# Kernel tuning notes

Measured on AMD Instinct MI355X. Metric: run time of the kernel, lower is better.

## Reference

```python
import jax, jax.numpy as jnp
import numpy as np

B, S, D, H, K, L, NS, NT = 32, 512, 1024, 512, 16, 16, 16, 16
SMOOTH = 0.1
EPS = 1e-8


def setup_inputs() -> dict:
    key = jax.random.key(0)
    ks = jax.random.split(key, 16)
    hidden_layers = jax.random.normal(ks[0], (B, S, D), jnp.float32)
    span_start = jax.random.randint(ks[1], (B, K), 0, S - L).astype(jnp.int32)
    span_idx = span_start[..., None] + jnp.arange(L, dtype=jnp.int32)  # [B,K,L] in-range
    span_mask = jnp.ones((B, K, L), jnp.float32)
    span_end = span_start + (L - 1)
    length = jnp.full((B,), S, jnp.int32)
    slot_emb = jax.random.normal(ks[2], (B, K, D), jnp.float32)
    tgt_slot_embs = jax.random.normal(ks[3], (NT, D), jnp.float32)
    src_slot_ids = jax.random.randint(ks[4], (B, K), 0, NS).astype(jnp.int32)
    sc = 0.02
    p = {
        'Wih_f': jax.random.normal(ks[5], (4 * H, D)) * sc,
        'Whh_f': jax.random.normal(ks[6], (4 * H, H)) * sc,
        'bih_f': jnp.zeros((4 * H,)), 'bhh_f': jnp.zeros((4 * H,)),
        'Wih_b': jax.random.normal(ks[7], (4 * H, D)) * sc,
        'Whh_b': jax.random.normal(ks[8], (4 * H, H)) * sc,
        'bih_b': jnp.zeros((4 * H,)), 'bhh_b': jnp.zeros((4 * H,)),
        # slot_name_projection_for_slot / _for_context are eye-initialized with zero bias
        'Wps1': jnp.eye(D), 'bps1': jnp.zeros((D,)),
        'Wps2': jnp.eye(D), 'bps2': jnp.zeros((D,)),
        'Wpc1': jnp.eye(D), 'bpc1': jnp.zeros((D,)),
        'Wpc2': jnp.eye(D), 'bpc2': jnp.zeros((D,)),
    }
    inp = dict(hidden_layers=hidden_layers, span_idx=span_idx, span_mask=span_mask,
               span_start=span_start, span_end=span_end, length=length,
               slot_emb=slot_emb, tgt_slot_embs=tgt_slot_embs, src_slot_ids=src_slot_ids)
    inp.update(p)
    return inp


def _lstm_dir(x, m, Wih, Whh, bih, bhh):
    # x: [N,L,D], m: [N,L]; masked steps carry state through, emit 0
    N = x.shape[0]
    h0 = jnp.zeros((N, H), x.dtype)
    c0 = jnp.zeros((N, H), x.dtype)

    def step(carry, xm):
        h, c = carry
        xt, mt = xm
        g = xt @ Wih.T + h @ Whh.T + (bih + bhh)
        i, f, gg, o = jnp.split(g, 4, axis=-1)  # torch gate order i,f,g,o
        cn = jax.nn.sigmoid(f) * c + jax.nn.sigmoid(i) * jnp.tanh(gg)
        hn = jax.nn.sigmoid(o) * jnp.tanh(cn)
        mt = mt[:, None]
        h = mt * hn + (1.0 - mt) * h
        c = mt * cn + (1.0 - mt) * c
        return (h, c), h * mt

    _, ys = jax.lax.scan(step, (h0, c0), (jnp.swapaxes(x, 0, 1), m.T))
    return jnp.swapaxes(ys, 0, 1)  # [N,L,H]


def _mlp(x, W1, b1, W2, b2):
    # Linear -> Tanh -> (Dropout eval=identity) -> Linear
    return jnp.tanh(x @ W1.T + b1) @ W2.T + b2


def reference(hidden_layers, span_idx, span_mask, span_start, span_end, length,
              slot_emb, tgt_slot_embs, src_slot_ids,
              Wih_f, Whh_f, bih_f, bhh_f, Wih_b, Whh_b, bih_b, bhh_b,
              Wps1, bps1, Wps2, bps2, Wpc1, bpc1, Wpc2, bpc2):
    # gather span tokens: [B,K,L,D]
    spans = hidden_layers[jnp.arange(B)[:, None, None], span_idx]
    x = spans.reshape(B * K, L, D)
    m = span_mask.reshape(B * K, L)
    hf = _lstm_dir(x, m, Wih_f, Whh_f, bih_f, bhh_f)
    hb = _lstm_dir(x[:, ::-1], m[:, ::-1], Wih_b, Whh_b, bih_b, bhh_b)[:, ::-1]
    out = jnp.concatenate([hf, hb], axis=-1)           # [BK,L,2H]
    slot_feats = out.sum(axis=1).reshape(B, K, 2 * H)  # sum-pool over span

    # context attention (faithful to source: returns attn @ hidden, no softmax)
    sf = jax.lax.stop_gradient(slot_feats)
    pos = jnp.arange(S)
    cmask = (pos[None, None, :] < span_start[..., None]) | \
            ((pos[None, None, :] > span_end[..., None]) & (pos[None, None, :] < length[:, None, None]))
    attn = jnp.einsum('bkd,bsd->bks', sf, hidden_layers) * cmask.astype(hidden_layers.dtype)
    context = jnp.einsum('bks,bsd->bkd', attn, hidden_layers)  # [B,K,D]

    # smooth labels via projected slot-name embeddings (all detached in source)
    s_cat = jnp.concatenate([_mlp(slot_emb, Wps1, bps1, Wps2, bps2),
                             _mlp(slot_emb, Wpc1, bpc1, Wpc2, bpc2)], axis=-1)  # [B,K,2D]
    t_cat = jnp.concatenate([_mlp(tgt_slot_embs, Wps1, bps1, Wps2, bps2),
                             _mlp(tgt_slot_embs, Wpc1, bpc1, Wpc2, bpc2)], axis=-1)  # [NT,2D]
    s_cat = jax.lax.stop_gradient(s_cat)
    t_cat = jax.lax.stop_gradient(t_cat)
    sn = jnp.maximum(jnp.linalg.norm(s_cat, axis=-1), EPS)
    tn = jnp.maximum(jnp.linalg.norm(t_cat, axis=-1), EPS)
    sim = jnp.einsum('bkd,td->bkt', s_cat, t_cat) / (sn[..., None] * tn[None, None, :])
    sim = sim / sim.sum(axis=-1, keepdims=True) * (1.0 - SMOOTH)
    one_hot = jax.nn.one_hot(src_slot_ids, NS, dtype=sim.dtype) * SMOOTH
    labels = jnp.concatenate([one_hot, sim], axis=-1)  # [B,K,NS+NT]

    return jnp.concatenate([slot_feats, context, labels], axis=-1)  # [B,K,2H+D+NS+NT]
```

## Files before the change

kernel.cpp:

```cpp
#include <hip/hip_runtime.h>
#include <cstdio>

#define B_ 32
#define S_ 512
#define D_ 1024
#define H_ 512
#define K_ 16
#define L_ 16
#define NT_ 16
#define NSEQ 512
#define XROWS 8192
#define G4H 2048
#define OUTC 2080
#define MROWS 528

typedef unsigned short u16;
typedef __bf16 bf16x8 __attribute__((ext_vector_type(8)));
typedef float f32x4 __attribute__((ext_vector_type(4)));

__device__ inline u16 f2b(float f) {
  union { float f; unsigned u; } x; x.f = f;
  unsigned r = x.u + 0x7FFFu + ((x.u >> 16) & 1u);
  return (u16)(r >> 16);
}
__device__ inline float b2f(u16 h) {
  union { unsigned u; float f; } c; c.u = ((unsigned)h) << 16;
  return c.f;
}
__device__ inline float sigf(float x) { return 1.0f / (1.0f + expf(-x)); }
__device__ inline float wredsum(float v) {
#pragma unroll
  for (int off = 32; off > 0; off >>= 1) v += __shfl_xor(v, off);
  return v;
}

__global__ __launch_bounds__(256) void split_kernel(const float* __restrict__ in,
                                                    u16* __restrict__ hi,
                                                    u16* __restrict__ lo, int n) {
  int i = blockIdx.x * 256 + threadIdx.x;
  if (i >= n) return;
  float x = in[i];
  u16 h = f2b(x);
  hi[i] = h;
  lo[i] = f2b(x - b2f(h));
}

__global__ __launch_bounds__(256) void hsplit_kernel(const float* __restrict__ in,
                                                     u16* __restrict__ hi,
                                                     u16* __restrict__ lo) {
  size_t i = ((size_t)blockIdx.x * 256 + threadIdx.x) * 4;
  float4 v = *reinterpret_cast<const float4*>(in + i);
  float a[4] = {v.x, v.y, v.z, v.w};
#pragma unroll
  for (int j = 0; j < 4; ++j) {
    u16 h = f2b(a[j]);
    hi[i + j] = h;
    lo[i + j] = f2b(a[j] - b2f(h));
  }
}

__global__ __launch_bounds__(256) void icast_kernel(const float* __restrict__ W,
                                                    u16* __restrict__ out, int Kd) {
  int rp = blockIdx.x;
  int j = rp >> 2, g = rp & 3;
  const float* src = W + ((size_t)(g * H_ + j)) * Kd;
  u16* dst = out + (size_t)rp * Kd;
  for (int k = threadIdx.x; k < Kd; k += 256) dst[k] = f2b(src[k]);
}

__global__ __launch_bounds__(256) void bsum_kernel(const float* __restrict__ bih,
                                                   const float* __restrict__ bhh,
                                                   float* __restrict__ bsum) {
  int rp = blockIdx.x * 256 + threadIdx.x;
  if (rp >= G4H) return;
  int j = rp >> 2, g = rp & 3;
  bsum[rp] = bih[g * H_ + j] + bhh[g * H_ + j];
}

__global__ __launch_bounds__(256) void gather_cast_kernel(const float* __restrict__ hidden,
                                                          const int* __restrict__ span_idx,
                                                          u16* __restrict__ Xbf) {
  int row = blockIdx.x;
  int n = row >> 4;
  int b = n >> 4;
  int s = span_idx[row];
  const float* src = hidden + ((size_t)b * S_ + s) * D_;
  u16* dst = Xbf + (size_t)row * D_;
  for (int d = threadIdx.x; d < D_; d += 256) dst[d] = f2b(src[d]);
}

__global__ __launch_bounds__(256) void gemm_bt_kernel(
    const u16* __restrict__ A, const u16* __restrict__ Bm,
    float* __restrict__ Cf, u16* __restrict__ Cb,
    int M, int N, int Kd, int ldc) {
  __shared__ u16 As[128][34];
  __shared__ u16 Bs[128][34];
  const int tid = threadIdx.x;
  const int bm = blockIdx.y * 128, bn = blockIdx.x * 128;
  const int wave = tid >> 6, lane = tid & 63;
  const int wm = (wave >> 1) * 64, wn = (wave & 1) * 64;
  f32x4 acc[4][4] = {};
  const int lr = tid >> 2;
  const int lk = (tid & 3) * 8;
  const int fr = lane & 15;
  const int kg = (lane >> 4) * 8;

  for (int k0 = 0; k0 < Kd; k0 += 32) {
#pragma unroll
    for (int half = 0; half < 2; ++half) {
      int row = lr + half * 64;
      uint4 va = {0u, 0u, 0u, 0u};
      int ga = bm + row;
      if (ga < M) va = *reinterpret_cast<const uint4*>(A + (size_t)ga * Kd + k0 + lk);
      *reinterpret_cast<uint4*>(&As[row][lk]) = va;
      uint4 vb = {0u, 0u, 0u, 0u};
      int gb = bn + row;
      if (gb < N) vb = *reinterpret_cast<const uint4*>(Bm + (size_t)gb * Kd + k0 + lk);
      *reinterpret_cast<uint4*>(&Bs[row][lk]) = vb;
    }
    __syncthreads();
    bf16x8 af[4], bfr[4];
#pragma unroll
    for (int m = 0; m < 4; ++m)
      af[m] = *reinterpret_cast<const bf16x8*>(&As[wm + m * 16 + fr][kg]);
#pragma unroll
    for (int n = 0; n < 4; ++n)
      bfr[n] = *reinterpret_cast<const bf16x8*>(&Bs[wn + n * 16 + fr][kg]);
#pragma unroll
    for (int m = 0; m < 4; ++m)
#pragma unroll
      for (int n = 0; n < 4; ++n)
        acc[m][n] = __builtin_amdgcn_mfma_f32_16x16x32_bf16(af[m], bfr[n], acc[m][n], 0, 0, 0);
    __syncthreads();
  }
  const int ci = lane & 15;
  const int r0 = (lane >> 4) * 4;
#pragma unroll
  for (int m = 0; m < 4; ++m)
#pragma unroll
    for (int n = 0; n < 4; ++n) {
      int col = bn + wn + n * 16 + ci;
#pragma unroll
      for (int r = 0; r < 4; ++r) {
        int row = bm + wm + m * 16 + r0 + r;
        if (row < M && col < N) {
          size_t idx = (size_t)row * ldc + col;
          if (Cb) Cb[idx] = f2b(acc[m][n][r]);
          else Cf[idx] = acc[m][n][r];
        }
      }
    }
}

__global__ __launch_bounds__(256) void lstm_step_kernel(
    const u16* __restrict__ hbf_in,
    const u16* __restrict__ Whhf, const u16* __restrict__ Whhb,
    const u16* __restrict__ G2,
    const float* __restrict__ bsumf, const float* __restrict__ bsumb,
    const float* __restrict__ mask,
    float* __restrict__ hst, float* __restrict__ cst,
    u16* __restrict__ hbf_out,
    float* __restrict__ sf,
    int t, int first) {
  __shared__ u16 As[64][34];
  __shared__ u16 Bs[64][34];
  const int tid = threadIdx.x;
  const int bz = blockIdx.z;
  const int treal = bz ? (L_ - 1 - t) : t;
  const u16* Whh = bz ? Whhb : Whhf;
  const float* bsum = bz ? bsumb : bsumf;
  const size_t sofs = (size_t)bz * NSEQ * H_;
  const int bm = blockIdx.y * 64, bn = blockIdx.x * 64;
  const int wave = tid >> 6, lane = tid & 63;
  const int wm = (wave >> 1) * 32, wn = (wave & 1) * 32;
  f32x4 acc[2][2] = {};
  const int lr = tid >> 2;
  const int lk = (tid & 3) * 8;
  const int fr = lane & 15;
  const int kg = (lane >> 4) * 8;

  if (!first) {
    for (int k0 = 0; k0 < H_; k0 += 32) {
      *reinterpret_cast<uint4*>(&As[lr][lk]) =
          *reinterpret_cast<const uint4*>(hbf_in + sofs + (size_t)(bm + lr) * H_ + k0 + lk);
      *reinterpret_cast<uint4*>(&Bs[lr][lk]) =
          *reinterpret_cast<const uint4*>(Whh + (size_t)(bn + lr) * H_ + k0 + lk);
      __syncthreads();
      bf16x8 af[2], bfr[2];
#pragma unroll
      for (int m = 0; m < 2; ++m)
        af[m] = *reinterpret_cast<const bf16x8*>(&As[wm + m * 16 + fr][kg]);
#pragma unroll
      for (int n = 0; n < 2; ++n)
        bfr[n] = *reinterpret_cast<const bf16x8*>(&Bs[wn + n * 16 + fr][kg]);
#pragma unroll
      for (int m = 0; m < 2; ++m)
#pragma unroll
        for (int n = 0; n < 2; ++n)
          acc[m][n] = __builtin_amdgcn_mfma_f32_16x16x32_bf16(af[m], bfr[n], acc[m][n], 0, 0, 0);
      __syncthreads();
    }
  }

  const int ci = lane & 15;
  const int r0 = (lane >> 4) * 4;
  const int q = lane & 3;
#pragma unroll
  for (int m = 0; m < 2; ++m)
#pragma unroll
    for (int n = 0; n < 2; ++n) {
      int c = bn + wn + n * 16 + ci;
      int rowbase = bm + wm + m * 16 + r0;
      float val[4];
#pragma unroll
      for (int r = 0; r < 4; ++r) {
        int nrow = rowbase + r;
        float g2 = b2f(G2[((size_t)nrow * L_ + treal) * 4096 + (size_t)bz * 2048 + c]);
        val[r] = acc[m][n][r] + g2 + bsum[c];
      }
      float x1[4], x2[4], x3[4];
#pragma unroll
      for (int r = 0; r < 4; ++r) {
        x1[r] = __shfl_xor(val[r], 1);
        x2[r] = __shfl_xor(val[r], 2);
        x3[r] = __shfl_xor(x1[r], 2);
      }
      if (q == 0) {
        int j = c >> 2;
#pragma unroll
        for (int r = 0; r < 4; ++r) {
          int nrow = rowbase + r;
          float gi = val[r], gf = x1[r], gg = x2[r], go = x3[r];
          float mv = mask[nrow * L_ + treal];
          size_t sidx = sofs + (size_t)nrow * H_ + j;
          float co = first ? 0.f : cst[sidx];
          float ho = first ? 0.f : hst[sidx];
          float cn = sigf(gf) * co + sigf(gi) * tanhf(gg);
          float hn = sigf(go) * tanhf(cn);
          float hnew = mv * hn + (1.f - mv) * ho;
          float cnew = mv * cn + (1.f - mv) * co;
          hst[sidx] = hnew;
          cst[sidx] = cnew;
          hbf_out[sidx] = f2b(hnew);
          size_t fidx = (size_t)nrow * 1024 + bz * 512 + j;
          float contrib = hnew * mv;
          if (first) sf[fidx] = contrib;
          else sf[fidx] += contrib;
        }
      }
    }
}

__global__ __launch_bounds__(256) void copy_sf_split_kernel(const float* __restrict__ sf,
                                                            float* __restrict__ out,
                                                            u16* __restrict__ sfh,
                                                            u16* __restrict__ sfl) {
  int bk = blockIdx.x;
  for (int d = threadIdx.x; d < 1024; d += 256) {
    size_t i = (size_t)bk * 1024 + d;
    float v = sf[i];
    out[(size_t)bk * OUTC + d] = v;
    u16 h = f2b(v);
    sfh[i] = h;
    sfl[i] = f2b(v - b2f(h));
  }
}

__global__ __launch_bounds__(256) void attn_mfma_kernel(
    const u16* __restrict__ sfh, const u16* __restrict__ sfl,
    const u16* __restrict__ Hh, const u16* __restrict__ Hl,
    const int* __restrict__ sstart, const int* __restrict__ send,
    const int* __restrict__ len,
    u16* __restrict__ attn_h, u16* __restrict__ attn_l) {
  __shared__ u16 Bh[128][34];
  __shared__ u16 Bl[128][34];
  const int b = blockIdx.x;
  const int s0 = blockIdx.y * 128;
  const int tid = threadIdx.x;
  const int wave = tid >> 6, lane = tid & 63;
  const int fr = lane & 15;
  const int kg = (lane >> 4) * 8;
  f32x4 acc[2] = {};
  const int lr = tid >> 2;
  const int lk = (tid & 3) * 8;

  for (int k0 = 0; k0 < D_; k0 += 32) {
#pragma unroll
    for (int half = 0; half < 2; ++half) {
      int srow = half * 64 + lr;
      size_t goff = ((size_t)b * S_ + s0 + srow) * D_ + k0 + lk;
      *reinterpret_cast<uint4*>(&Bh[srow][lk]) = *reinterpret_cast<const uint4*>(Hh + goff);
      *reinterpret_cast<uint4*>(&Bl[srow][lk]) = *reinterpret_cast<const uint4*>(Hl + goff);
    }
    __syncthreads();
    size_t aoff = ((size_t)b * 16 + fr) * D_ + k0 + kg;
    bf16x8 ah = *reinterpret_cast<const bf16x8*>(sfh + aoff);
    bf16x8 al = *reinterpret_cast<const bf16x8*>(sfl + aoff);
#pragma unroll
    for (int nt = 0; nt < 2; ++nt) {
      bf16x8 bh = *reinterpret_cast<const bf16x8*>(&Bh[wave * 32 + nt * 16 + fr][kg]);
      bf16x8 bl = *reinterpret_cast<const bf16x8*>(&Bl[wave * 32 + nt * 16 + fr][kg]);
      acc[nt] = __builtin_amdgcn_mfma_f32_16x16x32_bf16(ah, bh, acc[nt], 0, 0, 0);
      acc[nt] = __builtin_amdgcn_mfma_f32_16x16x32_bf16(ah, bl, acc[nt], 0, 0, 0);
      acc[nt] = __builtin_amdgcn_mfma_f32_16x16x32_bf16(al, bh, acc[nt], 0, 0, 0);
    }
    __syncthreads();
  }
  const int ln = len[b];
#pragma unroll
  for (int nt = 0; nt < 2; ++nt) {
    int s = s0 + wave * 32 + nt * 16 + (lane & 15);
#pragma unroll
    for (int r = 0; r < 4; ++r) {
      int krow = (lane >> 4) * 4 + r;
      int bk = b * 16 + krow;
      int st = sstart[bk], en = send[bk];
      bool cm = (s < st) || ((s > en) && (s < ln));
      float v = cm ? acc[nt][r] : 0.f;
      u16 h = f2b(v);
      size_t idx = (size_t)bk * S_ + s;
      attn_h[idx] = h;
      attn_l[idx] = f2b(v - b2f(h));
    }
  }
}

__global__ __launch_bounds__(256) void ctx_mfma_kernel(
    const u16* __restrict__ attn_h, const u16* __restrict__ attn_l,
    const u16* __restrict__ Hh, const u16* __restrict__ Hl,
    float* __restrict__ out) {
  __shared__ u16 Th[128][34];
  __shared__ u16 Tl[128][34];
  const int b = blockIdx.x;
  const int d0 = blockIdx.y * 128;
  const int tid = threadIdx.x;
  const int wave = tid >> 6, lane = tid & 63;
  const int fr = lane & 15;
  const int kg = (lane >> 4) * 8;
  f32x4 acc[2] = {};

  for (int k0 = 0; k0 < S_; k0 += 32) {
#pragma unroll
    for (int pass = 0; pass < 2; ++pass) {
      int idx = pass * 256 + tid;
      int srow = idx >> 4;
      int dch = (idx & 15) * 8;
      size_t goff = ((size_t)b * S_ + k0 + srow) * D_ + d0 + dch;
      uint4 vh = *reinterpret_cast<const uint4*>(Hh + goff);
      uint4 vl = *reinterpret_cast<const uint4*>(Hl + goff);
      const u16* ph = reinterpret_cast<const u16*>(&vh);
      const u16* pl = reinterpret_cast<const u16*>(&vl);
#pragma unroll
      for (int i = 0; i < 8; ++i) {
        Th[dch + i][srow] = ph[i];
        Tl[dch + i][srow] = pl[i];
      }
    }
    __syncthreads();
    size_t aoff = ((size_t)b * 16 + fr) * S_ + k0 + kg;
    bf16x8 ah = *reinterpret_cast<const bf16x8*>(attn_h + aoff);
    bf16x8 al = *reinterpret_cast<const bf16x8*>(attn_l + aoff);
#pragma unroll
    for (int nt = 0; nt < 2; ++nt) {
      bf16x8 bh = *reinterpret_cast<const bf16x8*>(&Th[wave * 32 + nt * 16 + fr][kg]);
      bf16x8 bl = *reinterpret_cast<const bf16x8*>(&Tl[wave * 32 + nt * 16 + fr][kg]);
      acc[nt] = __builtin_amdgcn_mfma_f32_16x16x32_bf16(ah, bh, acc[nt], 0, 0, 0);
      acc[nt] = __builtin_amdgcn_mfma_f32_16x16x32_bf16(ah, bl, acc[nt], 0, 0, 0);
      acc[nt] = __builtin_amdgcn_mfma_f32_16x16x32_bf16(al, bh, acc[nt], 0, 0, 0);
    }
    __syncthreads();
  }
#pragma unroll
  for (int nt = 0; nt < 2; ++nt) {
    int d = d0 + wave * 32 + nt * 16 + (lane & 15);
#pragma unroll
    for (int r = 0; r < 4; ++r) {
      int krow = (lane >> 4) * 4 + r;
      out[((size_t)b * 16 + krow) * OUTC + 1024 + d] = acc[nt][r];
    }
  }
}

__global__ __launch_bounds__(256) void mlp_gemm_kernel(
    const u16* __restrict__ Ah, const u16* __restrict__ Al, int a_br_stride,
    const u16* __restrict__ B0h, const u16* __restrict__ B0l,
    const u16* __restrict__ B1h, const u16* __restrict__ B1l,
    float* __restrict__ P, int M) {
  __shared__ u16 Ash[64][34];
  __shared__ u16 Asl[64][34];
  __shared__ u16 Bsh[64][34];
  __shared__ u16 Bsl[64][34];
  const int tid = threadIdx.x;
  const int zz = blockIdx.z;
  const int br = zz >> 2, ks = zz & 3;
  const u16* Ah_ = Ah + (size_t)br * a_br_stride;
  const u16* Al_ = Al + (size_t)br * a_br_stride;
  const u16* Bh = br ? B1h : B0h;
  const u16* Bl = br ? B1l : B0l;
  const int bm = blockIdx.y * 64, bn = blockIdx.x * 64;
  const int wave = tid >> 6, lane = tid & 63;
  const int wm = (wave >> 1) * 32, wn = (wave & 1) * 32;
  f32x4 acc[2][2] = {};
  const int lr = tid >> 2;
  const int lk = (tid & 3) * 8;
  const int fr = lane & 15;
  const int kg = (lane >> 4) * 8;

  const int kbeg = ks * 256;
  for (int k0 = kbeg; k0 < kbeg + 256; k0 += 32) {
    int ga = bm + lr;
    uint4 vah = {0, 0, 0, 0}, vall = {0, 0, 0, 0};
    if (ga < M) {
      vah = *reinterpret_cast<const uint4*>(Ah_ + (size_t)ga * D_ + k0 + lk);
      vall = *reinterpret_cast<const uint4*>(Al_ + (size_t)ga * D_ + k0 + lk);
    }
    *reinterpret_cast<uint4*>(&Ash[lr][lk]) = vah;
    *reinterpret_cast<uint4*>(&Asl[lr][lk]) = vall;
    *reinterpret_cast<uint4*>(&Bsh[lr][lk]) =
        *reinterpret_cast<const uint4*>(Bh + (size_t)(bn + lr) * D_ + k0 + lk);
    *reinterpret_cast<uint4*>(&Bsl[lr][lk]) =
        *reinterpret_cast<const uint4*>(Bl + (size_t)(bn + lr) * D_ + k0 + lk);
    __syncthreads();
    bf16x8 afh[2], afl[2], bfh[2], bfl[2];
#pragma unroll
    for (int m = 0; m < 2; ++m) {
      afh[m] = *reinterpret_cast<const bf16x8*>(&Ash[wm + m * 16 + fr][kg]);
      afl[m] = *reinterpret_cast<const bf16x8*>(&Asl[wm + m * 16 + fr][kg]);
    }
#pragma unroll
    for (int n = 0; n < 2; ++n) {
      bfh[n] = *reinterpret_cast<const bf16x8*>(&Bsh[wn + n * 16 + fr][kg]);
      bfl[n] = *reinterpret_cast<const bf16x8*>(&Bsl[wn + n * 16 + fr][kg]);
    }
#pragma unroll
    for (int m = 0; m < 2; ++m)
#pragma unroll
      for (int n = 0; n < 2; ++n) {
        acc[m][n] = __builtin_amdgcn_mfma_f32_16x16x32_bf16(afh[m], bfh[n], acc[m][n], 0, 0, 0);
        acc[m][n] = __builtin_amdgcn_mfma_f32_16x16x32_bf16(afh[m], bfl[n], acc[m][n], 0, 0, 0);
        acc[m][n] = __builtin_amdgcn_mfma_f32_16x16x32_bf16(afl[m], bfh[n], acc[m][n], 0, 0, 0);
      }
    __syncthreads();
  }
  const int ci = lane & 15;
  const int r0 = (lane >> 4) * 4;
#pragma unroll
  for (int m = 0; m < 2; ++m)
#pragma unroll
    for (int n = 0; n < 2; ++n) {
      int col = bn + wn + n * 16 + ci;
#pragma unroll
      for (int r = 0; r < 4; ++r) {
        int row = bm + wm + m * 16 + r0 + r;
        if (row < M)
          P[((size_t)zz * MROWS + row) * D_ + col] = acc[m][n][r];
      }
    }
}

__global__ __launch_bounds__(256) void mlp_reduce_kernel(
    const float* __restrict__ P,
    const float* __restrict__ bias0, const float* __restrict__ bias1,
    u16* __restrict__ Oh, u16* __restrict__ Ol,
    float* __restrict__ Cf,
    int mode) {
  int i = blockIdx.x * 256 + threadIdx.x;
  int e = i * 4;
  const int per_br = MROWS * D_;
  int br = e / per_br;
  int rem = e - br * per_br;
  int row = rem >> 10;
  int col = rem & 1023;
  float4 s = {0.f, 0.f, 0.f, 0.f};
#pragma unroll
  for (int ks = 0; ks < 4; ++ks) {
    float4 v = *reinterpret_cast<const float4*>(
        P + ((size_t)(br * 4 + ks) * MROWS + row) * D_ + col);
    s.x += v.x; s.y += v.y; s.z += v.z; s.w += v.w;
  }
  const float* bias = br ? bias1 : bias0;
  s.x += bias[col]; s.y += bias[col + 1]; s.z += bias[col + 2]; s.w += bias[col + 3];
  if (mode == 0) {
    float a[4] = {tanhf(s.x), tanhf(s.y), tanhf(s.z), tanhf(s.w)};
    size_t o = (size_t)br * per_br + (size_t)row * D_ + col;
#pragma unroll
    for (int j = 0; j < 4; ++j) {
      u16 h = f2b(a[j]);
      Oh[o + j] = h;
      Ol[o + j] = f2b(a[j] - b2f(h));
    }
  } else {
    *reinterpret_cast<float4*>(Cf + (size_t)row * 2048 + br * 1024 + col) = s;
  }
}

__global__ __launch_bounds__(64) void labels_kernel(
    const float* __restrict__ s_cat, const float* __restrict__ t_cat,
    const int* __restrict__ src_ids, float* __restrict__ out) {
  int bk = blockIdx.x, lane = threadIdx.x;
  const float* srow = s_cat + (size_t)bk * 2048;
  float np = 0.f;
  float dots[16], tsq[16];
#pragma unroll
  for (int t = 0; t < 16; ++t) { dots[t] = 0.f; tsq[t] = 0.f; }
  for (int j = lane; j < 2048; j += 64) {
    float sv = srow[j];
    np += sv * sv;
#pragma unroll
    for (int t = 0; t < 16; ++t) {
      float tv = t_cat[t * 2048 + j];
      dots[t] += sv * tv;
      tsq[t] += tv * tv;
    }
  }
  np = wredsum(np);
#pragma unroll
  for (int t = 0; t < 16; ++t) { dots[t] = wredsum(dots[t]); tsq[t] = wredsum(tsq[t]); }
  float sn = fmaxf(sqrtf(np), 1e-8f);
  float ssum = 0.f;
  float sims[16];
#pragma unroll
  for (int t = 0; t < 16; ++t) {
    float tn = fmaxf(sqrtf(tsq[t]), 1e-8f);
    sims[t] = dots[t] / (sn * tn);
    ssum += sims[t];
  }
  float scale = 0.9f / ssum;
  if (lane < 16) {
    out[(size_t)bk * OUTC + 2064 + lane] = sims[lane] * scale;
  } else if (lane < 32) {
    int t2 = lane - 16;
    out[(size_t)bk * OUTC + 2048 + t2] = (src_ids[bk] == t2) ? 0.1f : 0.f;
  }
}

extern "C" void kernel_launch(void* const* d_in, const int* in_sizes, int n_in,
                              void* d_out, int out_size, void* d_ws, size_t ws_size,
                              hipStream_t stream) {
  const float* hidden    = (const float*)d_in[0];
  const int*   span_idx  = (const int*)d_in[1];
  const float* span_mask = (const float*)d_in[2];
  const int*   span_start= (const int*)d_in[3];
  const int*   span_end  = (const int*)d_in[4];
  const int*   length    = (const int*)d_in[5];
  const float* slot_emb  = (const float*)d_in[6];
  const float* tgt       = (const float*)d_in[7];
  const int*   src_ids   = (const int*)d_in[8];
  const float* Wih_f = (const float*)d_in[9];
  const float* Whh_f = (const float*)d_in[10];
  const float* bih_f = (const float*)d_in[11];
  const float* bhh_f = (const float*)d_in[12];
  const float* Wih_b = (const float*)d_in[13];
  const float* Whh_b = (const float*)d_in[14];
  const float* bih_b = (const float*)d_in[15];
  const float* bhh_b = (const float*)d_in[16];
  const float* Wps1 = (const float*)d_in[17];
  const float* bps1 = (const float*)d_in[18];
  const float* Wps2 = (const float*)d_in[19];
  const float* bps2 = (const float*)d_in[20];
  const float* Wpc1 = (const float*)d_in[21];
  const float* bpc1 = (const float*)d_in[22];
  const float* Wpc2 = (const float*)d_in[23];
  const float* bpc2 = (const float*)d_in[24];
  float* out = (float*)d_out;

  char* p = (char*)d_ws;
  auto alloc = [&](size_t bytes) -> void* {
    void* r = (void*)p;
    p += (bytes + 255) & ~(size_t)255;
    return r;
  };
  u16*   Xbf   = (u16*)alloc((size_t)XROWS * D_ * 2);
  char*  BIG   = (char*)alloc((size_t)2 * B_ * S_ * D_ * 2 + (1 << 20));
  float* hst   = (float*)alloc((size_t)2 * NSEQ * H_ * 4);
  float* cst   = (float*)alloc((size_t)2 * NSEQ * H_ * 4);
  u16*   hbfA  = (u16*)alloc((size_t)2 * NSEQ * H_ * 2);
  u16*   hbfB  = (u16*)alloc((size_t)2 * NSEQ * H_ * 2);
  float* sf    = (float*)alloc((size_t)NSEQ * 1024 * 4);
  u16*   sfh   = (u16*)alloc((size_t)NSEQ * 1024 * 2);
  u16*   sfl   = (u16*)alloc((size_t)NSEQ * 1024 * 2);
  u16*   attn_h= (u16*)alloc((size_t)NSEQ * S_ * 2);
  u16*   attn_l= (u16*)alloc((size_t)NSEQ * S_ * 2);
  float* CAT   = (float*)alloc((size_t)MROWS * 2048 * 4);
  u16* Wih2_i = (u16*)alloc((size_t)2 * G4H * D_ * 2);
  u16* Whhf_i = (u16*)alloc((size_t)G4H * H_ * 2);
  u16* Whhb_i = (u16*)alloc((size_t)G4H * H_ * 2);
  float* bsumf = (float*)alloc(G4H * 4);
  float* bsumb = (float*)alloc(G4H * 4);
  u16* W1sh = (u16*)alloc((size_t)D_ * D_ * 2); u16* W1sl = (u16*)alloc((size_t)D_ * D_ * 2);
  u16* W2sh = (u16*)alloc((size_t)D_ * D_ * 2); u16* W2sl = (u16*)alloc((size_t)D_ * D_ * 2);
  u16* W1ch = (u16*)alloc((size_t)D_ * D_ * 2); u16* W1cl = (u16*)alloc((size_t)D_ * D_ * 2);
  u16* W2ch = (u16*)alloc((size_t)D_ * D_ * 2); u16* W2cl = (u16*)alloc((size_t)D_ * D_ * 2);
  u16* SEh = (u16*)alloc((size_t)MROWS * D_ * 2); u16* SEl = (u16*)alloc((size_t)MROWS * D_ * 2);

  u16*   G2 = (u16*)BIG;
  u16*   Hh = (u16*)BIG;
  u16*   Hl = Hh + (size_t)B_ * S_ * D_;
  float* P  = (float*)BIG;
  u16*   T1h = Xbf;
  u16*   T1l = Xbf + (size_t)2 * MROWS * D_;

  size_t need = (size_t)(p - (char*)d_ws);
  if (need > ws_size) {
    fprintf(stderr, "kernel_launch: ws too small, need %zu have %zu\n", need, ws_size);
    return;
  }

  auto split = [&](const float* src, u16* hi, u16* lo, int n) {
    split_kernel<<<(n + 255) / 256, 256, 0, stream>>>(src, hi, lo, n);
  };

  icast_kernel<<<G4H, 256, 0, stream>>>(Wih_f, Wih2_i, D_);
  icast_kernel<<<G4H, 256, 0, stream>>>(Wih_b, Wih2_i + (size_t)G4H * D_, D_);
  icast_kernel<<<G4H, 256, 0, stream>>>(Whh_f, Whhf_i, H_);
  icast_kernel<<<G4H, 256, 0, stream>>>(Whh_b, Whhb_i, H_);
  bsum_kernel<<<8, 256, 0, stream>>>(bih_f, bhh_f, bsumf);
  bsum_kernel<<<8, 256, 0, stream>>>(bih_b, bhh_b, bsumb);
  split(Wps1, W1sh, W1sl, D_ * D_);
  split(Wps2, W2sh, W2sl, D_ * D_);
  split(Wpc1, W1ch, W1cl, D_ * D_);
  split(Wpc2, W2ch, W2cl, D_ * D_);
  split(slot_emb, SEh, SEl, NSEQ * D_);
  split(tgt, SEh + (size_t)NSEQ * D_, SEl + (size_t)NSEQ * D_, NT_ * D_);

  gather_cast_kernel<<<XROWS, 256, 0, stream>>>(hidden, span_idx, Xbf);

  {
    dim3 g(4096 / 128, XROWS / 128);
    gemm_bt_kernel<<<g, 256, 0, stream>>>(Xbf, Wih2_i, nullptr, G2, XROWS, 4096, D_, 4096);
  }

  for (int t = 0; t < L_; ++t) {
    const u16* hin = (t & 1) ? hbfA : hbfB;
    u16* hout = (t & 1) ? hbfB : hbfA;
    dim3 g(G4H / 64, NSEQ / 64, 2);
    lstm_step_kernel<<<g, 256, 0, stream>>>(hin, Whhf_i, Whhb_i, G2, bsumf, bsumb,
                                            span_mask, hst, cst, hout, sf,
                                            t, t == 0 ? 1 : 0);
  }

  copy_sf_split_kernel<<<NSEQ, 256, 0, stream>>>(sf, out, sfh, sfl);

  hsplit_kernel<<<(B_ * S_ * D_) / (4 * 256), 256, 0, stream>>>(hidden, Hh, Hl);

  {
    dim3 g(B_, S_ / 128);
    attn_mfma_kernel<<<g, 256, 0, stream>>>(sfh, sfl, Hh, Hl,
                                            span_start, span_end, length,
                                            attn_h, attn_l);
  }
  {
    dim3 g(B_, D_ / 128);
    ctx_mfma_kernel<<<g, 256, 0, stream>>>(attn_h, attn_l, Hh, Hl, out);
  }

  {
    dim3 g(D_ / 64, (MROWS + 63) / 64, 8);
    dim3 rg((2 * MROWS * D_) / (4 * 256));
    mlp_gemm_kernel<<<g, 256, 0, stream>>>(SEh, SEl, 0, W1sh, W1sl, W1ch, W1cl, P, MROWS);
    mlp_reduce_kernel<<<rg, 256, 0, stream>>>(P, bps1, bpc1, T1h, T1l, nullptr, 0);
    mlp_gemm_kernel<<<g, 256, 0, stream>>>(T1h, T1l, MROWS * D_, W2sh, W2sl, W2ch, W2cl, P, MROWS);
    mlp_reduce_kernel<<<rg, 256, 0, stream>>>(P, bps2, bpc2, nullptr, nullptr, CAT, 1);
  }

  const float* t_cat = CAT + (size_t)NSEQ * 2048;
  labels_kernel<<<NSEQ, 64, 0, stream>>>(CAT, t_cat, src_ids, out);
}
```

Before: 776.1 us.

## Use direct global-to-LDS loads and fuse span gather into input GEMM

```diff
diff --git a/kernel.cpp b/kernel.cpp
--- a/kernel.cpp
+++ b/kernel.cpp
@@ -33,6 +33,11 @@
   for (int off = 32; off > 0; off >>= 1) v += __shfl_xor(v, off);
   return v;
 }
+__device__ inline void gl16(const u16* g, u16* l) {
+  __builtin_amdgcn_global_load_lds(
+      (const __attribute__((address_space(1))) unsigned int*)g,
+      (__attribute__((address_space(3))) unsigned int*)l, 16, 0, 0);
+}
 
 __global__ __launch_bounds__(256) void split_kernel(const float* __restrict__ in,
                                                     u16* __restrict__ hi,
@@ -77,55 +82,49 @@
   bsum[rp] = bih[g * H_ + j] + bhh[g * H_ + j];
 }
 
-__global__ __launch_bounds__(256) void gather_cast_kernel(const float* __restrict__ hidden,
-                                                          const int* __restrict__ span_idx,
-                                                          u16* __restrict__ Xbf) {
-  int row = blockIdx.x;
-  int n = row >> 4;
-  int b = n >> 4;
-  int s = span_idx[row];
-  const float* src = hidden + ((size_t)b * S_ + s) * D_;
-  u16* dst = Xbf + (size_t)row * D_;
-  for (int d = threadIdx.x; d < D_; d += 256) dst[d] = f2b(src[d]);
-}
-
-__global__ __launch_bounds__(256) void gemm_bt_kernel(
-    const u16* __restrict__ A, const u16* __restrict__ Bm,
-    float* __restrict__ Cf, u16* __restrict__ Cb,
-    int M, int N, int Kd, int ldc) {
-  __shared__ u16 As[128][34];
-  __shared__ u16 Bs[128][34];
+__global__ __launch_bounds__(256) void big_gemm_kernel(
+    const u16* __restrict__ Hh, const int* __restrict__ span_idx,
+    const u16* __restrict__ Wih2, u16* __restrict__ G2) {
+  __shared__ u16 As[128 * 32];
+  __shared__ u16 Bs[128 * 32];
   const int tid = threadIdx.x;
-  const int bm = blockIdx.y * 128, bn = blockIdx.x * 128;
+  const int bn = blockIdx.x * 128, bm = blockIdx.y * 128;
   const int wave = tid >> 6, lane = tid & 63;
   const int wm = (wave >> 1) * 64, wn = (wave & 1) * 64;
-  f32x4 acc[4][4] = {};
-  const int lr = tid >> 2;
-  const int lk = (tid & 3) * 8;
   const int fr = lane & 15;
   const int kg = (lane >> 4) * 8;
 
-  for (int k0 = 0; k0 < Kd; k0 += 32) {
-#pragma unroll
-    for (int half = 0; half < 2; ++half) {
-      int row = lr + half * 64;
-      uint4 va = {0u, 0u, 0u, 0u};
-      int ga = bm + row;
-      if (ga < M) va = *reinterpret_cast<const uint4*>(A + (size_t)ga * Kd + k0 + lk);
-      *reinterpret_cast<uint4*>(&As[row][lk]) = va;
-      uint4 vb = {0u, 0u, 0u, 0u};
-      int gb = bn + row;
-      if (gb < N) vb = *reinterpret_cast<const uint4*>(Bm + (size_t)gb * Kd + k0 + lk);
-      *reinterpret_cast<uint4*>(&Bs[row][lk]) = vb;
-    }
+  const u16* asrc[2];
+  const u16* bsrc[2];
+  u16* adst[2];
+  u16* bdst[2];
+#pragma unroll
+  for (int j = 0; j < 2; ++j) {
+    int c = tid + 256 * j;
+    int gr = bm + (c >> 2);
+    int b = gr >> 8;
+    int sidx = span_idx[gr];
+    asrc[j] = Hh + ((size_t)(b * S_ + sidx)) * D_ + (c & 3) * 8;
+    bsrc[j] = Wih2 + (size_t)(bn + (c >> 2)) * D_ + (c & 3) * 8;
+    int ub = (wave * 64 + 256 * j) * 8;
+    adst[j] = As + ub;
+    bdst[j] = Bs + ub;
+  }
+
+  f32x4 acc[4][4] = {};
+  for (int k0 = 0; k0 < D_; k0 += 32) {
+    gl16(asrc[0] + k0, adst[0]);
+    gl16(asrc[1] + k0, adst[1]);
+    gl16(bsrc[0] + k0, bdst[0]);
+    gl16(bsrc[1] + k0, bdst[1]);
     __syncthreads();
     bf16x8 af[4], bfr[4];
 #pragma unroll
     for (int m = 0; m < 4; ++m)
-      af[m] = *reinterpret_cast<const bf16x8*>(&As[wm + m * 16 + fr][kg]);
+      af[m] = *reinterpret_cast<const bf16x8*>(&As[(wm + m * 16 + fr) * 32 + kg]);
 #pragma unroll
     for (int n = 0; n < 4; ++n)
-      bfr[n] = *reinterpret_cast<const bf16x8*>(&Bs[wn + n * 16 + fr][kg]);
+      bfr[n] = *reinterpret_cast<const bf16x8*>(&Bs[(wn + n * 16 + fr) * 32 + kg]);
 #pragma unroll
     for (int m = 0; m < 4; ++m)
 #pragma unroll
@@ -143,11 +142,7 @@
 #pragma unroll
       for (int r = 0; r < 4; ++r) {
         int row = bm + wm + m * 16 + r0 + r;
-        if (row < M && col < N) {
-          size_t idx = (size_t)row * ldc + col;
-          if (Cb) Cb[idx] = f2b(acc[m][n][r]);
-          else Cf[idx] = acc[m][n][r];
-        }
+        G2[(size_t)row * 4096 + col] = f2b(acc[m][n][r]);
       }
     }
 }
@@ -162,8 +157,8 @@
     u16* __restrict__ hbf_out,
     float* __restrict__ sf,
     int t, int first) {
-  __shared__ u16 As[64][34];
-  __shared__ u16 Bs[64][34];
+  __shared__ u16 As[64 * 32];
+  __shared__ u16 Bs[64 * 32];
   const int tid = threadIdx.x;
   const int bz = blockIdx.z;
   const int treal = bz ? (L_ - 1 - t) : t;
@@ -174,25 +169,26 @@
   const int wave = tid >> 6, lane = tid & 63;
   const int wm = (wave >> 1) * 32, wn = (wave & 1) * 32;
   f32x4 acc[2][2] = {};
-  const int lr = tid >> 2;
-  const int lk = (tid & 3) * 8;
   const int fr = lane & 15;
   const int kg = (lane >> 4) * 8;
 
   if (!first) {
+    const int c = tid;
+    const u16* asrc = hbf_in + sofs + (size_t)(bm + (c >> 2)) * H_ + (c & 3) * 8;
+    const u16* bsrc = Whh + (size_t)(bn + (c >> 2)) * H_ + (c & 3) * 8;
+    u16* adst = As + wave * 512;
+    u16* bdst = Bs + wave * 512;
     for (int k0 = 0; k0 < H_; k0 += 32) {
-      *reinterpret_cast<uint4*>(&As[lr][lk]) =
-          *reinterpret_cast<const uint4*>(hbf_in + sofs + (size_t)(bm + lr) * H_ + k0 + lk);
-      *reinterpret_cast<uint4*>(&Bs[lr][lk]) =
-          *reinterpret_cast<const uint4*>(Whh + (size_t)(bn + lr) * H_ + k0 + lk);
+      gl16(asrc + k0, adst);
+      gl16(bsrc + k0, bdst);
       __syncthreads();
       bf16x8 af[2], bfr[2];
 #pragma unroll
       for (int m = 0; m < 2; ++m)
-        af[m] = *reinterpret_cast<const bf16x8*>(&As[wm + m * 16 + fr][kg]);
+        af[m] = *reinterpret_cast<const bf16x8*>(&As[(wm + m * 16 + fr) * 32 + kg]);
 #pragma unroll
       for (int n = 0; n < 2; ++n)
-        bfr[n] = *reinterpret_cast<const bf16x8*>(&Bs[wn + n * 16 + fr][kg]);
+        bfr[n] = *reinterpret_cast<const bf16x8*>(&Bs[(wn + n * 16 + fr) * 32 + kg]);
 #pragma unroll
       for (int m = 0; m < 2; ++m)
 #pragma unroll
@@ -272,8 +268,8 @@
     const int* __restrict__ sstart, const int* __restrict__ send,
     const int* __restrict__ len,
     u16* __restrict__ attn_h, u16* __restrict__ attn_l) {
-  __shared__ u16 Bh[128][34];
-  __shared__ u16 Bl[128][34];
+  __shared__ u16 Bh[128 * 32];
+  __shared__ u16 Bl[128 * 32];
   const int b = blockIdx.x;
   const int s0 = blockIdx.y * 128;
   const int tid = threadIdx.x;
@@ -281,25 +277,35 @@
   const int fr = lane & 15;
   const int kg = (lane >> 4) * 8;
   f32x4 acc[2] = {};
-  const int lr = tid >> 2;
-  const int lk = (tid & 3) * 8;
+
+  const u16* hsrc[2];
+  const u16* lsrc[2];
+  u16* hdst[2];
+  u16* ldst[2];
+#pragma unroll
+  for (int j = 0; j < 2; ++j) {
+    int c = tid + 256 * j;
+    size_t goff = ((size_t)b * S_ + s0 + (c >> 2)) * D_ + (c & 3) * 8;
+    hsrc[j] = Hh + goff;
+    lsrc[j] = Hl + goff;
+    int ub = (wave * 64 + 256 * j) * 8;
+    hdst[j] = Bh + ub;
+    ldst[j] = Bl + ub;
+  }
 
   for (int k0 = 0; k0 < D_; k0 += 32) {
-#pragma unroll
-    for (int half = 0; half < 2; ++half) {
-      int srow = half * 64 + lr;
-      size_t goff = ((size_t)b * S_ + s0 + srow) * D_ + k0 + lk;
-      *reinterpret_cast<uint4*>(&Bh[srow][lk]) = *reinterpret_cast<const uint4*>(Hh + goff);
-      *reinterpret_cast<uint4*>(&Bl[srow][lk]) = *reinterpret_cast<const uint4*>(Hl + goff);
-    }
+    gl16(hsrc[0] + k0, hdst[0]);
+    gl16(hsrc[1] + k0, hdst[1]);
+    gl16(lsrc[0] + k0, ldst[0]);
+    gl16(lsrc[1] + k0, ldst[1]);
     __syncthreads();
     size_t aoff = ((size_t)b * 16 + fr) * D_ + k0 + kg;
     bf16x8 ah = *reinterpret_cast<const bf16x8*>(sfh + aoff);
     bf16x8 al = *reinterpret_cast<const bf16x8*>(sfl + aoff);
 #pragma unroll
     for (int nt = 0; nt < 2; ++nt) {
-      bf16x8 bh = *reinterpret_cast<const bf16x8*>(&Bh[wave * 32 + nt * 16 + fr][kg]);
-      bf16x8 bl = *reinterpret_cast<const bf16x8*>(&Bl[wave * 32 + nt * 16 + fr][kg]);
+      bf16x8 bh = *reinterpret_cast<const bf16x8*>(&Bh[(wave * 32 + nt * 16 + fr) * 32 + kg]);
+      bf16x8 bl = *reinterpret_cast<const bf16x8*>(&Bl[(wave * 32 + nt * 16 + fr) * 32 + kg]);
       acc[nt] = __builtin_amdgcn_mfma_f32_16x16x32_bf16(ah, bh, acc[nt], 0, 0, 0);
       acc[nt] = __builtin_amdgcn_mfma_f32_16x16x32_bf16(ah, bl, acc[nt], 0, 0, 0);
       acc[nt] = __builtin_amdgcn_mfma_f32_16x16x32_bf16(al, bh, acc[nt], 0, 0, 0);
@@ -386,10 +392,10 @@
     const u16* __restrict__ B0h, const u16* __restrict__ B0l,
     const u16* __restrict__ B1h, const u16* __restrict__ B1l,
     float* __restrict__ P, int M) {
-  __shared__ u16 Ash[64][34];
-  __shared__ u16 Asl[64][34];
-  __shared__ u16 Bsh[64][34];
-  __shared__ u16 Bsl[64][34];
+  __shared__ u16 Ash[64 * 32];
+  __shared__ u16 Asl[64 * 32];
+  __shared__ u16 Bsh[64 * 32];
+  __shared__ u16 Bsl[64 * 32];
   const int tid = threadIdx.x;
   const int zz = blockIdx.z;
   const int br = zz >> 2, ks = zz & 3;
@@ -401,36 +407,38 @@
   const int wave = tid >> 6, lane = tid & 63;
   const int wm = (wave >> 1) * 32, wn = (wave & 1) * 32;
   f32x4 acc[2][2] = {};
-  const int lr = tid >> 2;
-  const int lk = (tid & 3) * 8;
   const int fr = lane & 15;
   const int kg = (lane >> 4) * 8;
 
+  const int c = tid;
+  int ga = bm + (c >> 2);
+  if (ga >= M) ga = M - 1;
+  const u16* ahsrc = Ah_ + (size_t)ga * D_ + (c & 3) * 8;
+  const u16* alsrc = Al_ + (size_t)ga * D_ + (c & 3) * 8;
+  const u16* bhsrc = Bh + (size_t)(bn + (c >> 2)) * D_ + (c & 3) * 8;
+  const u16* blsrc = Bl + (size_t)(bn + (c >> 2)) * D_ + (c & 3) * 8;
+  u16* d0 = Ash + wave * 512;
+  u16* d1 = Asl + wave * 512;
+  u16* d2 = Bsh + wave * 512;
+  u16* d3 = Bsl + wave * 512;
+
   const int kbeg = ks * 256;
   for (int k0 = kbeg; k0 < kbeg + 256; k0 += 32) {
-    int ga = bm + lr;
-    uint4 vah = {0, 0, 0, 0}, vall = {0, 0, 0, 0};
-    if (ga < M) {
-      vah = *reinterpret_cast<const uint4*>(Ah_ + (size_t)ga * D_ + k0 + lk);
-      vall = *reinterpret_cast<const uint4*>(Al_ + (size_t)ga * D_ + k0 + lk);
-    }
-    *reinterpret_cast<uint4*>(&Ash[lr][lk]) = vah;
-    *reinterpret_cast<uint4*>(&Asl[lr][lk]) = vall;
-    *reinterpret_cast<uint4*>(&Bsh[lr][lk]) =
-        *reinterpret_cast<const uint4*>(Bh + (size_t)(bn + lr) * D_ + k0 + lk);
-    *reinterpret_cast<uint4*>(&Bsl[lr][lk]) =
-        *reinterpret_cast<const uint4*>(Bl + (size_t)(bn + lr) * D_ + k0 + lk);
+    gl16(ahsrc + k0, d0);
+    gl16(alsrc + k0, d1);
+    gl16(bhsrc + k0, d2);
+    gl16(blsrc + k0, d3);
     __syncthreads();
     bf16x8 afh[2], afl[2], bfh[2], bfl[2];
 #pragma unroll
     for (int m = 0; m < 2; ++m) {
-      afh[m] = *reinterpret_cast<const bf16x8*>(&Ash[wm + m * 16 + fr][kg]);
-      afl[m] = *reinterpret_cast<const bf16x8*>(&Asl[wm + m * 16 + fr][kg]);
+      afh[m] = *reinterpret_cast<const bf16x8*>(&Ash[(wm + m * 16 + fr) * 32 + kg]);
+      afl[m] = *reinterpret_cast<const bf16x8*>(&Asl[(wm + m * 16 + fr) * 32 + kg]);
     }
 #pragma unroll
     for (int n = 0; n < 2; ++n) {
-      bfh[n] = *reinterpret_cast<const bf16x8*>(&Bsh[wn + n * 16 + fr][kg]);
-      bfl[n] = *reinterpret_cast<const bf16x8*>(&Bsl[wn + n * 16 + fr][kg]);
+      bfh[n] = *reinterpret_cast<const bf16x8*>(&Bsh[(wn + n * 16 + fr) * 32 + kg]);
+      bfl[n] = *reinterpret_cast<const bf16x8*>(&Bsl[(wn + n * 16 + fr) * 32 + kg]);
     }
 #pragma unroll
     for (int m = 0; m < 2; ++m)
@@ -570,8 +578,8 @@
     p += (bytes + 255) & ~(size_t)255;
     return r;
   };
-  u16*   Xbf   = (u16*)alloc((size_t)XROWS * D_ * 2);
-  char*  BIG   = (char*)alloc((size_t)2 * B_ * S_ * D_ * 2 + (1 << 20));
+  char*  BIG1  = (char*)alloc((size_t)XROWS * 4096 * 2);
+  char*  BIG2  = (char*)alloc((size_t)2 * B_ * S_ * D_ * 2);
   float* hst   = (float*)alloc((size_t)2 * NSEQ * H_ * 4);
   float* cst   = (float*)alloc((size_t)2 * NSEQ * H_ * 4);
   u16*   hbfA  = (u16*)alloc((size_t)2 * NSEQ * H_ * 2);
@@ -592,13 +600,13 @@
   u16* W1ch = (u16*)alloc((size_t)D_ * D_ * 2); u16* W1cl = (u16*)alloc((size_t)D_ * D_ * 2);
   u16* W2ch = (u16*)alloc((size_t)D_ * D_ * 2); u16* W2cl = (u16*)alloc((size_t)D_ * D_ * 2);
   u16* SEh = (u16*)alloc((size_t)MROWS * D_ * 2); u16* SEl = (u16*)alloc((size_t)MROWS * D_ * 2);
-
-  u16*   G2 = (u16*)BIG;
-  u16*   Hh = (u16*)BIG;
+  u16* T1h = (u16*)alloc((size_t)2 * MROWS * D_ * 2);
+  u16* T1l = (u16*)alloc((size_t)2 * MROWS * D_ * 2);
+
+  u16*   G2 = (u16*)BIG1;
+  float* P  = (float*)BIG1;
+  u16*   Hh = (u16*)BIG2;
   u16*   Hl = Hh + (size_t)B_ * S_ * D_;
-  float* P  = (float*)BIG;
-  u16*   T1h = Xbf;
-  u16*   T1l = Xbf + (size_t)2 * MROWS * D_;
 
   size_t need = (size_t)(p - (char*)d_ws);
   if (need > ws_size) {
@@ -623,11 +631,11 @@
   split(slot_emb, SEh, SEl, NSEQ * D_);
   split(tgt, SEh + (size_t)NSEQ * D_, SEl + (size_t)NSEQ * D_, NT_ * D_);
 
-  gather_cast_kernel<<<XROWS, 256, 0, stream>>>(hidden, span_idx, Xbf);
+  hsplit_kernel<<<(B_ * S_ * D_) / (4 * 256), 256, 0, stream>>>(hidden, Hh, Hl);
 
   {
     dim3 g(4096 / 128, XROWS / 128);
-    gemm_bt_kernel<<<g, 256, 0, stream>>>(Xbf, Wih2_i, nullptr, G2, XROWS, 4096, D_, 4096);
+    big_gemm_kernel<<<g, 256, 0, stream>>>(Hh, span_idx, Wih2_i, G2);
   }
 
   for (int t = 0; t < L_; ++t) {
@@ -641,8 +649,6 @@
 
   copy_sf_split_kernel<<<NSEQ, 256, 0, stream>>>(sf, out, sfh, sfl);
 
-  hsplit_kernel<<<(B_ * S_ * D_) / (4 * 256), 256, 0, stream>>>(hidden, Hh, Hl);
-
   {
     dim3 g(B_, S_ / 128);
     attn_mfma_kernel<<<g, 256, 0, stream>>>(sfh, sfl, Hh, Hl,
```

Measured after the change: 633.2 us. -18.4%, faster.
